# Kernel tuning notes

Hardware: AMD Instinct MI355X
Metric: run time of the kernel (lower is better)

The kernel has to match this reference:

```python
import jax, jax.numpy as jnp
import numpy as np

B, N, F, T, O, K = 4, 4000, 16, 16, 16, 3
LN_EPS = 1e-5


def setup_inputs() -> dict:
    key = jax.random.key(0)
    k = jax.random.split(key, 18)
    rn = lambda i, sh, sc=1.0: jax.random.normal(k[i], sh, dtype=jnp.float32) * np.float32(sc)
    ru = lambda i, sh: jax.random.uniform(k[i], sh, dtype=jnp.float32)
    return {
        "x": rn(0, (B, N, F, T)),
        # scale the random Laplacian so the Chebyshev recurrence stays numerically sane
        "laplacian": rn(1, (N, N), 1.0 / np.sqrt(N)),
        "W1": ru(2, (T,)),
        "W2": rn(3, (F, T)),
        "W3": ru(4, (F,)),
        "bs": ru(5, (1, N, N)),
        "Vs": ru(6, (N, N)),
        "U1": ru(7, (N,)),
        "U2": rn(8, (F, N)),
        "U3": ru(9, (F,)),
        "be": ru(10, (1, T, T)),
        "Ve": ru(11, (T, T)),
        "cheb_w": rn(12, (K, F, O), 1.0 / np.sqrt(F)),
        "time_w": rn(13, (O, F, T), 1.0 / np.sqrt(F * T)),
        "time_b": rn(14, (O,)),
        "ln_g": jnp.ones((N, O), dtype=jnp.float32),
        "ln_b": jnp.zeros((N, O), dtype=jnp.float32),
    }


def reference(x, laplacian, W1, W2, W3, bs, Vs, U1, U2, U3, be, Ve,
              cheb_w, time_w, time_b, ln_g, ln_b):
    # ---- temporal attention: E (B,T,T) ----
    # lhs[b,t] = sum_{n,f} x[b,n,f,t] * U1[n]
    t_lhs = jnp.einsum('bnft,n->bt', x, U1)
    # rhs[b,t] = sum_{n,f,g} x[b,n,f,t] * U2[g,n] * U3[g]
    t_rhs = jnp.einsum('bnft,gn,g->bt', x, U2, U3)
    t_prod = t_lhs[:, :, None] * t_rhs[:, None, :]          # (B,T,T) outer product
    E = jnp.einsum('ts,bsr->btr', Ve, jax.nn.sigmoid(t_prod + be))
    E = jax.nn.softmax(E, axis=-1)

    # apply temporal attention along the time axis: (B,N,F,T)
    x_TAt = jnp.einsum('bts,bnfs->bnft', E, x)

    # ---- spatial attention: S (B,N,N) ----
    s_lhs = jnp.einsum('bnft,t->bnf', x, W1)                 # (B,N,F)
    # faithful to the source ops (valid since F == T here)
    s_rhs = jnp.einsum('bnkt,gk,t->bng', x, W2, W3)          # (B,N,F)
    s_prod = jnp.einsum('bnf,bmf->bnm', s_lhs, s_rhs)        # (B,N,N)
    S = jnp.einsum('nm,bmk->bnk', Vs, jax.nn.sigmoid(s_prod + bs))
    S = jax.nn.softmax(S, axis=-1)

    # spatially attended features for all timesteps at once
    x_SAtt = jnp.einsum('bnm,bmft->bnft', S, x_TAt)          # (B,N,F,T)

    # ---- Chebyshev graph conv over every timestep ----
    Tx0 = x_SAtt
    out = jnp.einsum('bnft,fo->bnot', Tx0, cheb_w[0])
    Tx1 = jnp.einsum('nm,bmft->bnft', laplacian, Tx0)
    out = out + jnp.einsum('bnft,fo->bnot', Tx1, cheb_w[1])
    for kk in range(2, K):
        Tx2 = 2.0 * jnp.einsum('nm,bmft->bnft', laplacian, Tx1) - Tx0
        out = out + jnp.einsum('bnft,fo->bnot', Tx2, cheb_w[kk])
        Tx0, Tx1 = Tx1, Tx2
    spatial_gcn_avg = out.mean(axis=-1)                      # (B,N,O)

    # ---- time conv: Conv2d(in,out,kernel=(1,T)) == full contraction over (F,T) ----
    time_out = jnp.einsum('bnct,oct->bno', x, time_w) + time_b

    # ---- residual (in_channels == out_channels branch) ----
    residual = x[:, :, :, -1]                                # (B,N,O)

    y = spatial_gcn_avg + time_out + residual
    # LayerNorm over the last two dims [N, O]
    mean = y.mean(axis=(1, 2), keepdims=True)
    var = jnp.var(y, axis=(1, 2), keepdims=True)
    y = (y - mean) / jnp.sqrt(var + LN_EPS) * ln_g + ln_b
    return jax.nn.relu(y)
```

## Files before the change

### kernel.cpp

```cpp
#include <hip/hip_runtime.h>
#include <math.h>

#define Bc 4
#define Nn 4000
#define KS 4096
#define NP (16000000 + 4096)

typedef _Float16 half8 __attribute__((ext_vector_type(8)));
typedef float f32x4 __attribute__((ext_vector_type(4)));
typedef unsigned short u16x4 __attribute__((ext_vector_type(4)));

static __device__ __forceinline__ unsigned short f2h(float f) {
  _Float16 h = (_Float16)f;
  unsigned short u;
  __builtin_memcpy(&u, &h, 2);
  return u;
}
static __device__ __forceinline__ float h2f(unsigned short u) {
  _Float16 h;
  __builtin_memcpy(&h, &u, 2);
  return (float)h;
}
static __device__ __forceinline__ void gld16(const void* g, void* l) {
  __builtin_amdgcn_global_load_lds(
      (const __attribute__((address_space(1))) unsigned int*)g,
      (__attribute__((address_space(3))) unsigned int*)l, 16, 0, 0);
}

__global__ __launch_bounds__(256) void k1_trhs(
    const float* __restrict__ x, const float* __restrict__ U1,
    const float* __restrict__ U2, const float* __restrict__ U3,
    float* __restrict__ tl, float* __restrict__ tr) {
  int b = blockIdx.y;
  int tid = threadIdx.x;
  int q = tid & 3;
  int n = blockIdx.x * 64 + (tid >> 2);
  float xs[16];
#pragma unroll
  for (int t = 0; t < 16; ++t) xs[t] = 0.f;
  float c1 = 0.f, c2 = 0.f;
  if (n < Nn) {
    const float* xr = x + ((size_t)b * Nn + n) * 256 + q * 64;
#pragma unroll
    for (int f = 0; f < 4; ++f) {
#pragma unroll
      for (int qq = 0; qq < 4; ++qq) {
        float4 v = *(const float4*)(xr + f * 16 + qq * 4);
        xs[qq * 4 + 0] += v.x; xs[qq * 4 + 1] += v.y;
        xs[qq * 4 + 2] += v.z; xs[qq * 4 + 3] += v.w;
      }
    }
    c1 = U1[n];
#pragma unroll
    for (int g = 0; g < 4; ++g) {
      int gg = q * 4 + g;
      c2 += U2[(size_t)gg * Nn + n] * U3[gg];
    }
  }
#pragma unroll
  for (int m = 1; m < 4; m <<= 1) {
    c2 += __shfl_xor(c2, m, 64);
#pragma unroll
    for (int t = 0; t < 16; ++t) xs[t] += __shfl_xor(xs[t], m, 64);
  }
  float v1[4], v2[4];
#pragma unroll
  for (int i = 0; i < 4; ++i) {
    int t = q * 4 + i;
    v1[i] = c1 * xs[t];
    v2[i] = c2 * xs[t];
  }
#pragma unroll
  for (int off = 4; off < 64; off <<= 1) {
#pragma unroll
    for (int i = 0; i < 4; ++i) {
      v1[i] += __shfl_down(v1[i], off, 64);
      v2[i] += __shfl_down(v2[i], off, 64);
    }
  }
  int lane = tid & 63;
  if (lane < 4) {
#pragma unroll
    for (int i = 0; i < 4; ++i) {
      atomicAdd(&tl[b * 16 + lane * 4 + i], v1[i]);
      atomicAdd(&tr[b * 16 + lane * 4 + i], v2[i]);
    }
  }
}

__global__ __launch_bounds__(256) void k2_eattn(
    const float* __restrict__ tl, const float* __restrict__ tr,
    const float* __restrict__ be, const float* __restrict__ Ve,
    float* __restrict__ ecol) {
  int b = blockIdx.x;
  int tid = threadIdx.x;
  __shared__ float sig[256];
  __shared__ float Em[256];
  int s = tid >> 4, r = tid & 15;
  float z = tl[b * 16 + s] * tr[b * 16 + r] + be[s * 16 + r];
  sig[s * 16 + r] = 1.0f / (1.0f + __expf(-z));
  __syncthreads();
  float e = 0.f;
#pragma unroll
  for (int ss = 0; ss < 16; ++ss) e += Ve[s * 16 + ss] * sig[ss * 16 + r];
  Em[s * 16 + r] = e;
  __syncthreads();
  if (tid < 16) {
    float m = -1e30f;
#pragma unroll
    for (int rr = 0; rr < 16; ++rr) m = fmaxf(m, Em[tid * 16 + rr]);
    float ssum = 0.f;
    float ex[16];
#pragma unroll
    for (int rr = 0; rr < 16; ++rr) { ex[rr] = __expf(Em[tid * 16 + rr] - m); ssum += ex[rr]; }
    float inv = 1.0f / ssum;
#pragma unroll
    for (int rr = 0; rr < 16; ++rr) Em[tid * 16 + rr] = ex[rr] * inv;
  }
  __syncthreads();
  if (tid < 16) {
    float c = 0.f;
#pragma unroll
    for (int tt = 0; tt < 16; ++tt) c += Em[tt * 16 + tid];
    ecol[b * 16 + tid] = c;
  }
}

__global__ __launch_bounds__(256) void k3_pern(
    const float* __restrict__ x, const float* __restrict__ ecol,
    const float* __restrict__ W1, const float* __restrict__ W2,
    const float* __restrict__ W3, const float* __restrict__ time_w,
    const float* __restrict__ time_b,
    float* __restrict__ xts, float* __restrict__ slhs,
    float* __restrict__ srhs, float* __restrict__ base) {
  __shared__ float tws[4096];
  __shared__ float W1s[16], W3s[16], Ecs[16], tbs[16], W2s[256];
  int tid = threadIdx.x;
  int b = blockIdx.y;
  for (int i = tid; i < 4096; i += 256) tws[i] = time_w[i];
  W2s[tid] = W2[tid & 255];
  if (tid < 16) {
    W1s[tid] = W1[tid]; W3s[tid] = W3[tid];
    Ecs[tid] = ecol[b * 16 + tid]; tbs[tid] = time_b[tid];
  }
  __syncthreads();
  int n = blockIdx.x * 256 + tid;
  if (n >= Nn) return;
  const float* xr = x + ((size_t)b * Nn + n) * 256;
  float xtsv[16], slv[16], xw3[16], to[16], resid[16];
#pragma unroll
  for (int i = 0; i < 16; ++i) { xtsv[i] = 0; slv[i] = 0; xw3[i] = 0; to[i] = 0; }
  for (int f = 0; f < 16; ++f) {
    float xf[16];
#pragma unroll
    for (int q = 0; q < 4; ++q) {
      float4 v = *(const float4*)(xr + f * 16 + q * 4);
      xf[q * 4 + 0] = v.x; xf[q * 4 + 1] = v.y; xf[q * 4 + 2] = v.z; xf[q * 4 + 3] = v.w;
    }
    float a = 0, c = 0, d = 0;
#pragma unroll
    for (int t2 = 0; t2 < 16; ++t2) {
      a += Ecs[t2] * xf[t2];
      c += W1s[t2] * xf[t2];
      d += W3s[t2] * xf[t2];
    }
    xtsv[f] = a; slv[f] = c; xw3[f] = d; resid[f] = xf[15];
#pragma unroll
    for (int o = 0; o < 16; ++o) {
      float acc = 0;
#pragma unroll
      for (int t2 = 0; t2 < 16; ++t2) acc += tws[o * 256 + f * 16 + t2] * xf[t2];
      to[o] += acc;
    }
  }
  size_t o16 = ((size_t)b * Nn + n) * 16;
#pragma unroll
  for (int g = 0; g < 16; ++g) {
    float acc = 0;
#pragma unroll
    for (int k2 = 0; k2 < 16; ++k2) acc += W2s[g * 16 + k2] * xw3[k2];
    srhs[o16 + g] = acc;
  }
#pragma unroll
  for (int i = 0; i < 16; ++i) {
    xts[o16 + i] = xtsv[i];
    slhs[o16 + i] = slv[i];
    base[o16 + i] = to[i] + tbs[i] + resid[i];
  }
}

__global__ __launch_bounds__(256) void fconv(
    const float* __restrict__ src, unsigned short* __restrict__ dst) {
  size_t i = ((size_t)blockIdx.x * 256 + threadIdx.x) * 4;
  float4 v = *(const float4*)(src + i);
  u16x4 h;
  h.x = f2h(v.x); h.y = f2h(v.y); h.z = f2h(v.z); h.w = f2h(v.w);
  *(u16x4*)(dst + i) = h;
}

__global__ __launch_bounds__(256) void vconv2(
    const float* __restrict__ Vs, unsigned short* __restrict__ Vh) {
  int row = blockIdx.y;
  int col = blockIdx.x * 1024 + threadIdx.x * 4;
  u16x4 h;
  if (row < Nn && col < Nn) {
    float4 v = *(const float4*)(Vs + (size_t)row * Nn + col);
    h.x = f2h(v.x); h.y = f2h(v.y); h.z = f2h(v.z); h.w = f2h(v.w);
  } else {
    h.x = 0; h.y = 0; h.z = 0; h.w = 0;
  }
  *(u16x4*)(Vh + (size_t)row * KS + col) = h;
}

__global__ __launch_bounds__(256) void tsconv(
    const float* __restrict__ ts, unsigned short* __restrict__ tsT) {
  int n = blockIdx.x * 256 + threadIdx.x;
  int col = blockIdx.y;
  if (n >= Nn) return;
  int b = col >> 4, f = col & 15;
  tsT[(size_t)col * Nn + n] = f2h(ts[((size_t)b * Nn + n) * 16 + f]);
}

__global__ __launch_bounds__(256) void gemm1_P(
    const float* __restrict__ slhs, const float* __restrict__ srhs,
    const unsigned short* __restrict__ bsH, unsigned short* __restrict__ PhT, int b) {
  __shared__ float Ms[64][17];
  __shared__ float Cs[64][17];
  __shared__ float Pt[64][65];
  int tid = threadIdx.x;
  int m0 = blockIdx.y * 64, k0 = blockIdx.x * 64;
  int lr = tid >> 2, lq = (tid & 3) << 2;
  {
    int gm = m0 + lr; if (gm > Nn - 1) gm = Nn - 1;
    float4 v = *(const float4*)(slhs + ((size_t)b * Nn + gm) * 16 + lq);
    Ms[lr][lq + 0] = v.x; Ms[lr][lq + 1] = v.y; Ms[lr][lq + 2] = v.z; Ms[lr][lq + 3] = v.w;
    int gk = k0 + lr; if (gk > Nn - 1) gk = Nn - 1;
    float4 w = *(const float4*)(srhs + ((size_t)b * Nn + gk) * 16 + lq);
    Cs[lr][lq + 0] = w.x; Cs[lr][lq + 1] = w.y; Cs[lr][lq + 2] = w.z; Cs[lr][lq + 3] = w.w;
  }
  __syncthreads();
  int tx = tid & 15, ty = tid >> 4;
  float acc[4][4] = {};
#pragma unroll
  for (int f = 0; f < 16; ++f) {
    float a4[4], b4[4];
#pragma unroll
    for (int i = 0; i < 4; ++i) a4[i] = Ms[ty * 4 + i][f];
#pragma unroll
    for (int j = 0; j < 4; ++j) b4[j] = Cs[tx * 4 + j][f];
#pragma unroll
    for (int i = 0; i < 4; ++i)
#pragma unroll
      for (int j = 0; j < 4; ++j) acc[i][j] += a4[i] * b4[j];
  }
#pragma unroll
  for (int i = 0; i < 4; ++i) {
    int m = m0 + ty * 4 + i;
    int k = k0 + tx * 4;
    float bv[4] = {0.f, 0.f, 0.f, 0.f};
    if (m < Nn) {
      if (k + 3 < Nn) {
        u16x4 t4 = *(const u16x4*)(bsH + (size_t)m * Nn + k);
        bv[0] = h2f(t4.x); bv[1] = h2f(t4.y); bv[2] = h2f(t4.z); bv[3] = h2f(t4.w);
      } else {
        for (int j = 0; j < 4; ++j)
          if (k + j < Nn) bv[j] = h2f(bsH[(size_t)m * Nn + k + j]);
      }
    }
#pragma unroll
    for (int j = 0; j < 4; ++j) {
      float z = acc[i][j] + bv[j];
      Pt[ty * 4 + i][tx * 4 + j] = 1.f / (1.f + __expf(-z));
    }
  }
  __syncthreads();
#pragma unroll
  for (int i = 0; i < 4; ++i) {
    int kl = ty * 4 + i;
    int ml = tx * 4;
    int gm = m0 + ml;
    u16x4 h;
    h.x = f2h(Pt[ml + 0][kl]);
    h.y = f2h(Pt[ml + 1][kl]);
    h.z = f2h(Pt[ml + 2][kl]);
    h.w = f2h(Pt[ml + 3][kl]);
    size_t off = (size_t)(k0 + kl) * KS + gm;
    if (gm + 3 < Nn) {
      *(u16x4*)(PhT + off) = h;
    } else {
      unsigned short hv[4] = {h.x, h.y, h.z, h.w};
      for (int q = 0; q < 4; ++q)
        if (gm + q < Nn) PhT[off + q] = hv[q];
    }
  }
}

__global__ __launch_bounds__(512, 2) void gemm2_mfma(
    const unsigned short* __restrict__ Vh, const unsigned short* __restrict__ PhT,
    float* __restrict__ SP, unsigned int* __restrict__ rmaxu) {
  __shared__ unsigned short Ah[2][2][8192];
  __shared__ unsigned short Bh[2][2][8192];
  int t = threadIdx.x;
  int bid = blockIdx.x;
  int wg = (bid & 7) * 32 + (bid >> 3);
  int row0 = (wg >> 4) * 256, col0 = (wg & 15) * 256;

  int sr = t >> 2, sg = t & 3;
  int ssw = sg ^ ((t >> 3) & 3);
  size_t a0 = (size_t)(row0 + sr) * KS + ssw * 8;
  size_t a1 = (size_t)(row0 + 128 + sr) * KS + ssw * 8;
  size_t b0 = (size_t)(col0 + sr) * KS + ssw * 8;
  size_t b1 = (size_t)(col0 + 128 + sr) * KS + ssw * 8;
  int ld0 = t * 8, ld1 = 4096 + t * 8;

  int lane = t & 63, wid = t >> 6;
  int wm = (wid >> 2) * 128, wn = (wid & 3) * 64;
  int ml = lane & 15, qd = lane >> 4;
  int gr = qd ^ ((ml >> 1) & 3);
  int aro[8], bro[4];
#pragma unroll
  for (int i = 0; i < 8; ++i) aro[i] = (wm + ml + i * 16) * 32 + gr * 8;
#pragma unroll
  for (int j = 0; j < 4; ++j) bro[j] = (wn + ml + j * 16) * 32 + gr * 8;

  f32x4 acc[8][4] = {};

#define STG(P, X, bf, kh, o0, o1, kt)                          \
  do {                                                         \
    size_t c_ = (size_t)(kt) * 64 + (kh) * 32;                 \
    gld16(P + (o0) + c_, &X[bf][kh][ld0]);                     \
    gld16(P + (o1) + c_, &X[bf][kh][ld1]);                     \
  } while (0)
#define LGKM0() asm volatile("s_waitcnt lgkmcnt(0)" ::: "memory")
#define VM8()   asm volatile("s_waitcnt vmcnt(8)" ::: "memory")
#define BARR()  __builtin_amdgcn_s_barrier()

  STG(Vh, Ah, 0, 0, a0, a1, 0); STG(PhT, Bh, 0, 0, b0, b1, 0);
  STG(Vh, Ah, 0, 1, a0, a1, 0); STG(PhT, Bh, 0, 1, b0, b1, 0);
  STG(Vh, Ah, 1, 0, a0, a1, 1); STG(PhT, Bh, 1, 0, b0, b1, 1);
  STG(Vh, Ah, 1, 1, a0, a1, 1); STG(PhT, Bh, 1, 1, b0, b1, 1);
  asm volatile("s_waitcnt vmcnt(12)" ::: "memory");
  BARR();

#pragma unroll 1
  for (int G = 0; G < 64; ++G) {
    int cb = G & 1, nb = cb ^ 1;
    int tn1 = (G + 1 < 64) ? G + 1 : 63;
    int tn2 = (G + 2 < 64) ? G + 2 : 63;
    half8 av[4], bv[4];
#pragma unroll
    for (int j = 0; j < 4; ++j) bv[j] = *(const half8*)&Bh[cb][0][bro[j]];
#pragma unroll
    for (int i = 0; i < 4; ++i) av[i] = *(const half8*)&Ah[cb][0][aro[i]];
    STG(Vh, Ah, nb, 1, a0, a1, tn1);
    __builtin_amdgcn_s_setprio(1);
#pragma unroll
    for (int i = 0; i < 4; ++i)
#pragma unroll
      for (int j = 0; j < 4; ++j)
        acc[i][j] = __builtin_amdgcn_mfma_f32_16x16x32_f16(av[i], bv[j], acc[i][j], 0, 0, 0);
    __builtin_amdgcn_s_setprio(0);
    LGKM0();
    BARR();
#pragma unroll
    for (int i = 0; i < 4; ++i) av[i] = *(const half8*)&Ah[cb][0][aro[4 + i]];
    STG(PhT, Bh, nb, 1, b0, b1, tn1);
    __builtin_amdgcn_s_setprio(1);
#pragma unroll
    for (int i = 0; i < 4; ++i)
#pragma unroll
      for (int j = 0; j < 4; ++j)
        acc[4 + i][j] = __builtin_amdgcn_mfma_f32_16x16x32_f16(av[i], bv[j], acc[4 + i][j], 0, 0, 0);
    __builtin_amdgcn_s_setprio(0);
    LGKM0();
    VM8();
    BARR();
#pragma unroll
    for (int j = 0; j < 4; ++j) bv[j] = *(const half8*)&Bh[cb][1][bro[j]];
#pragma unroll
    for (int i = 0; i < 4; ++i) av[i] = *(const half8*)&Ah[cb][1][aro[i]];
    STG(Vh, Ah, cb, 0, a0, a1, tn2);
    __builtin_amdgcn_s_setprio(1);
#pragma unroll
    for (int i = 0; i < 4; ++i)
#pragma unroll
      for (int j = 0; j < 4; ++j)
        acc[i][j] = __builtin_amdgcn_mfma_f32_16x16x32_f16(av[i], bv[j], acc[i][j], 0, 0, 0);
    __builtin_amdgcn_s_setprio(0);
    LGKM0();
    BARR();
#pragma unroll
    for (int i = 0; i < 4; ++i) av[i] = *(const half8*)&Ah[cb][1][aro[4 + i]];
    STG(PhT, Bh, cb, 0, b0, b1, tn2);
    __builtin_amdgcn_s_setprio(1);
#pragma unroll
    for (int i = 0; i < 4; ++i)
#pragma unroll
      for (int j = 0; j < 4; ++j)
        acc[4 + i][j] = __builtin_amdgcn_mfma_f32_16x16x32_f16(av[i], bv[j], acc[4 + i][j], 0, 0, 0);
    __builtin_amdgcn_s_setprio(0);
    LGKM0();
    VM8();
    BARR();
  }
#undef STG
#undef LGKM0
#undef VM8
#undef BARR

#pragma unroll
  for (int i = 0; i < 8; ++i) {
#pragma unroll
    for (int r = 0; r < 4; ++r) {
      int grow = row0 + wm + i * 16 + qd * 4 + r;
      if (grow >= Nn) continue;
      float rowmax = -3.0e38f;
#pragma unroll
      for (int j = 0; j < 4; ++j) {
        int gcol = col0 + wn + j * 16 + ml;
        if (gcol < Nn) {
          float v = acc[i][j][r];
          SP[(size_t)grow * Nn + gcol] = v;
          rowmax = fmaxf(rowmax, v);
        }
      }
#pragma unroll
      for (int mk = 1; mk < 16; mk <<= 1)
        rowmax = fmaxf(rowmax, __shfl_xor(rowmax, mk, 64));
      if (ml == 0) {
        unsigned u = __float_as_uint(rowmax);
        u = (u & 0x80000000u) ? ~u : (u | 0x80000000u);
        atomicMax(rmaxu + grow, u);
      }
    }
  }
}

__global__ __launch_bounds__(256) void txsum_sp(
    const float* __restrict__ SP, const float* __restrict__ xts,
    const unsigned int* __restrict__ rmaxu, float* __restrict__ lsum,
    float* __restrict__ ts0, int b) {
  __shared__ unsigned short XT[16][824];
  int tid = threadIdx.x;
  int kbase = blockIdx.y * 800;
  for (int i4 = tid; i4 < 3200; i4 += 256) {
    int k = i4 >> 2, f4 = (i4 & 3) << 2;
    float4 v = *(const float4*)(xts + ((size_t)b * Nn + kbase + k) * 16 + f4);
    XT[f4 + 0][k] = f2h(v.x); XT[f4 + 1][k] = f2h(v.y);
    XT[f4 + 2][k] = f2h(v.z); XT[f4 + 3][k] = f2h(v.w);
  }
  __syncthreads();
  int lane = tid & 63, wid = tid >> 6;
  int ml = lane & 15, qd = lane >> 4;
  int n0 = blockIdx.x * 64 + wid * 16;
  int nr = n0 + ml;
  int nrc = nr < Nn ? nr : Nn - 1;
  unsigned u = rmaxu[nrc];
  u = (u & 0x80000000u) ? (u ^ 0x80000000u) : ~u;
  float rm = __uint_as_float(u);
  const float* spr = SP + (size_t)nrc * Nn + kbase + qd * 8;
  f32x4 acc = {0.f, 0.f, 0.f, 0.f};
  float lpart = 0.f;
#pragma unroll 1
  for (int ks = 0; ks < 25; ++ks) {
    float4 v0 = *(const float4*)(spr + ks * 32);
    float4 v1 = *(const float4*)(spr + ks * 32 + 4);
    float e0 = __expf(v0.x - rm), e1 = __expf(v0.y - rm);
    float e2 = __expf(v0.z - rm), e3 = __expf(v0.w - rm);
    float e4 = __expf(v1.x - rm), e5 = __expf(v1.y - rm);
    float e6 = __expf(v1.z - rm), e7 = __expf(v1.w - rm);
    lpart += ((e0 + e1) + (e2 + e3)) + ((e4 + e5) + (e6 + e7));
    half8 a_h, b_h;
    a_h[0] = (_Float16)e0; a_h[1] = (_Float16)e1;
    a_h[2] = (_Float16)e2; a_h[3] = (_Float16)e3;
    a_h[4] = (_Float16)e4; a_h[5] = (_Float16)e5;
    a_h[6] = (_Float16)e6; a_h[7] = (_Float16)e7;
    b_h = *(const half8*)&XT[ml][ks * 32 + qd * 8];
    acc = __builtin_amdgcn_mfma_f32_16x16x32_f16(a_h, b_h, acc, 0, 0, 0);
  }
  lpart += __shfl_xor(lpart, 16, 64);
  lpart += __shfl_xor(lpart, 32, 64);
  if (qd == 0 && nr < Nn) atomicAdd(&lsum[nr], lpart);
#pragma unroll
  for (int r = 0; r < 4; ++r) {
    int n = n0 + qd * 4 + r;
    if (n < Nn) atomicAdd(&ts0[((size_t)b * Nn + n) * 16 + ml], acc[r]);
  }
}

__global__ __launch_bounds__(256) void nrm_k(
    float* __restrict__ ts0, const float* __restrict__ lsum) {
  int tid = threadIdx.x;
  int b = blockIdx.y;
  int n = blockIdx.x * 16 + (tid >> 4);
  size_t i = ((size_t)b * Nn + n) * 16 + (tid & 15);
  ts0[i] = ts0[i] / lsum[b * Nn + n];
}

__global__ __launch_bounds__(256) void chebm(
    const unsigned short* __restrict__ lapH, const unsigned short* __restrict__ tsT,
    float* __restrict__ Cout) {
  __shared__ unsigned short Ah[64 * 32];
  __shared__ unsigned short Bh[64 * 32];
  int t = threadIdx.x;
  int row0 = blockIdx.x * 64;
  int kc0 = blockIdx.y * 25 * 32;
  int kc1 = kc0 + 25 * 32;
  int arow = row0 + (t >> 2); if (arow > Nn - 1) arow = Nn - 1;
  size_t a_base = (size_t)arow * Nn + (t & 3) * 8;
  size_t b_base = (size_t)(t >> 2) * Nn + (t & 3) * 8;

  int lane = t & 63;
  int wid = t >> 6;
  int wm = (wid >> 1) * 32, wn = (wid & 1) * 32;
  int ml = lane & 15, qd = lane >> 4;
  int aoff = (wm + ml) * 32 + qd * 8;
  int boff = (wn + ml) * 32 + qd * 8;

  f32x4 acc[2][2] = {};

  for (int k0 = kc0; k0 < kc1; k0 += 32) {
    gld16(lapH + a_base + k0, &Ah[t * 8]);
    gld16(tsT + b_base + k0, &Bh[t * 8]);
    __syncthreads();
    half8 a_h[2], b_h[2];
#pragma unroll
    for (int i = 0; i < 2; ++i) a_h[i] = *(const half8*)&Ah[aoff + i * 512];
#pragma unroll
    for (int j = 0; j < 2; ++j) b_h[j] = *(const half8*)&Bh[boff + j * 512];
#pragma unroll
    for (int i = 0; i < 2; ++i)
#pragma unroll
      for (int j = 0; j < 2; ++j)
        acc[i][j] = __builtin_amdgcn_mfma_f32_16x16x32_f16(a_h[i], b_h[j], acc[i][j], 0, 0, 0);
    __syncthreads();
  }
#pragma unroll
  for (int i = 0; i < 2; ++i)
#pragma unroll
    for (int j = 0; j < 2; ++j) {
      int gcol = wn + j * 16 + ml;
      int b = gcol >> 4, f = gcol & 15;
#pragma unroll
      for (int r = 0; r < 4; ++r) {
        int grow = row0 + wm + i * 16 + qd * 4 + r;
        if (grow < Nn) {
          size_t idx = ((size_t)b * Nn + grow) * 16 + f;
          atomicAdd(&Cout[idx], acc[i][j][r]);
        }
      }
    }
}

__global__ __launch_bounds__(256) void ky_k(
    const float* __restrict__ ts0, const float* __restrict__ ts1,
    const float* __restrict__ ts2, const float* __restrict__ cw,
    const float* __restrict__ base, float* __restrict__ ybuf,
    float* __restrict__ lnacc) {
  __shared__ float T0[256], T1[256], T2[256], CW[768];
  __shared__ float rs[256], rq[256];
  int tid = threadIdx.x;
  int b = blockIdx.y;
  size_t base_i = ((size_t)b * Nn + blockIdx.x * 16) * 16;
  T0[tid] = ts0[base_i + tid];
  T1[tid] = ts1[base_i + tid];
  T2[tid] = ts2[base_i + tid];
  for (int i = tid; i < 768; i += 256) CW[i] = cw[i];
  __syncthreads();
  int r = tid >> 4, o = tid & 15;
  float acc = 0.f;
#pragma unroll
  for (int f2 = 0; f2 < 16; ++f2) {
    float c2 = CW[512 + f2 * 16 + o];
    acc += T0[r * 16 + f2] * (CW[f2 * 16 + o] - c2);
    acc += T1[r * 16 + f2] * CW[256 + f2 * 16 + o];
    acc += (2.0f * T2[r * 16 + f2]) * c2;
  }
  float y = acc * 0.0625f + base[base_i + tid];
  ybuf[base_i + tid] = y;
  rs[tid] = y; rq[tid] = y * y;
  __syncthreads();
  for (int s2 = 128; s2 > 0; s2 >>= 1) {
    if (tid < s2) { rs[tid] += rs[tid + s2]; rq[tid] += rq[tid + s2]; }
    __syncthreads();
  }
  if (tid == 0) {
    atomicAdd(&lnacc[b * 2 + 0], rs[0]);
    atomicAdd(&lnacc[b * 2 + 1], rq[0]);
  }
}

__global__ __launch_bounds__(256) void kln_k(
    const float* __restrict__ ybuf, const float* __restrict__ lnacc,
    const float* __restrict__ lg, const float* __restrict__ lb,
    float* __restrict__ outp) {
  int tid = threadIdx.x;
  int b = blockIdx.y;
  size_t i = ((size_t)b * Nn + blockIdx.x * 16) * 16 + tid;
  size_t nz = (size_t)blockIdx.x * 256 + tid;
  const float inv = 1.0f / 64000.0f;
  float s = lnacc[b * 2 + 0], q = lnacc[b * 2 + 1];
  float mean = s * inv;
  float var = q * inv - mean * mean;
  float rstd = rsqrtf(var + 1e-5f);
  float v = (ybuf[i] - mean) * rstd * lg[nz] + lb[nz];
  outp[i] = fmaxf(v, 0.f);
}

extern "C" void kernel_launch(void* const* d_in, const int* in_sizes, int n_in,
                              void* d_out, int out_size, void* d_ws, size_t ws_size,
                              hipStream_t stream) {
  const float* x   = (const float*)d_in[0];
  const float* lap = (const float*)d_in[1];
  const float* W1  = (const float*)d_in[2];
  const float* W2  = (const float*)d_in[3];
  const float* W3  = (const float*)d_in[4];
  const float* bs  = (const float*)d_in[5];
  const float* Vs  = (const float*)d_in[6];
  const float* U1  = (const float*)d_in[7];
  const float* U2  = (const float*)d_in[8];
  const float* U3  = (const float*)d_in[9];
  const float* be  = (const float*)d_in[10];
  const float* Ve  = (const float*)d_in[11];
  const float* cw  = (const float*)d_in[12];
  const float* tw  = (const float*)d_in[13];
  const float* tb  = (const float*)d_in[14];
  const float* lg  = (const float*)d_in[15];
  const float* lb  = (const float*)d_in[16];
  float* ws = (float*)d_ws;
  float* SP = ws;
  unsigned short* Vh   = (unsigned short*)(ws + (size_t)NP);
  unsigned short* PhT  = Vh + (size_t)KS * KS;
  unsigned short* lapH = PhT + (size_t)KS * KS;
  unsigned short* bsH  = lapH + (size_t)Nn * Nn;
  unsigned short* tsT  = bsH + (size_t)Nn * Nn;
  float* xts  = (float*)(tsT + 64 * Nn + 64);
  float* slhs = xts + 256000;
  float* srhs = slhs + 256000;
  float* base = srhs + 256000;
  float* ts0  = base + 256000;
  float* ts1  = ts0 + 256000;
  float* ts2  = ts1 + 256000;
  float* ybuf = ts2 + 256000;
  float* tl   = ybuf + 256000;
  float* tr   = tl + 64;
  float* ecol = tr + 64;
  unsigned int* rmaxu = (unsigned int*)(ecol + 64);
  float* lsum = (float*)(rmaxu + Bc * Nn);
  float* lnacc = lsum + Bc * Nn;

  hipMemsetAsync(tl, 0, 128 * sizeof(float), stream);
  hipMemsetAsync(lnacc, 0, 8 * sizeof(float), stream);
  hipMemsetAsync(ts0, 0, 256000 * sizeof(float), stream);
  hipMemsetAsync(ts1, 0, 256000 * sizeof(float), stream);
  hipMemsetAsync(ts2, 0, 256000 * sizeof(float), stream);
  hipMemsetAsync(rmaxu, 0, Bc * Nn * sizeof(unsigned int), stream);
  hipMemsetAsync(lsum, 0, Bc * Nn * sizeof(float), stream);

  k1_trhs<<<dim3(63, 4), 256, 0, stream>>>(x, U1, U2, U3, tl, tr);
  k2_eattn<<<dim3(4), 256, 0, stream>>>(tl, tr, be, Ve, ecol);
  k3_pern<<<dim3(16, 4), 256, 0, stream>>>(x, ecol, W1, W2, W3, tw, tb,
                                           xts, slhs, srhs, base);
  vconv2<<<dim3(4, 4096), 256, 0, stream>>>(Vs, Vh);
  fconv<<<dim3(15625), 256, 0, stream>>>(lap, lapH);
  fconv<<<dim3(15625), 256, 0, stream>>>(bs, bsH);
  for (int b = 0; b < 4; ++b) {
    gemm1_P<<<dim3(63, 63), 256, 0, stream>>>(slhs, srhs, bsH, PhT, b);
    gemm2_mfma<<<dim3(256), 512, 0, stream>>>(Vh, PhT, SP, rmaxu + b * Nn);
    txsum_sp<<<dim3(63, 5), 256, 0, stream>>>(SP, xts, rmaxu + b * Nn,
                                              lsum + b * Nn, ts0, b);
  }
  nrm_k<<<dim3(250, 4), 256, 0, stream>>>(ts0, lsum);
  tsconv<<<dim3(16, 64), 256, 0, stream>>>(ts0, tsT);
  chebm<<<dim3(63, 5), 256, 0, stream>>>(lapH, tsT, ts1);
  tsconv<<<dim3(16, 64), 256, 0, stream>>>(ts1, tsT);
  chebm<<<dim3(63, 5), 256, 0, stream>>>(lapH, tsT, ts2);
  ky_k<<<dim3(250, 4), 256, 0, stream>>>(ts0, ts1, ts2, cw, base, ybuf, lnacc);
  kln_k<<<dim3(250, 4), 256, 0, stream>>>(ybuf, lnacc, lg, lb, (float*)d_out);
}
```

Measured before the change: 1.102 ms.

## Split per-node work across lanes, fuse conversions, double-buffer chebm loads

After: 1.074 ms. -2.5%, faster.

```diff
diff --git a/kernel.cpp b/kernel.cpp
--- a/kernel.cpp
+++ b/kernel.cpp
@@ -133,29 +133,36 @@
     const float* __restrict__ time_b,
     float* __restrict__ xts, float* __restrict__ slhs,
     float* __restrict__ srhs, float* __restrict__ base) {
-  __shared__ float tws[4096];
+  __shared__ float tws[16 * 272];
   __shared__ float W1s[16], W3s[16], Ecs[16], tbs[16], W2s[256];
   int tid = threadIdx.x;
   int b = blockIdx.y;
-  for (int i = tid; i < 4096; i += 256) tws[i] = time_w[i];
+  for (int i = tid; i < 4096; i += 256) {
+    int o = i >> 8, rem = i & 255, f = rem >> 4, t2 = rem & 15;
+    tws[o * 272 + f * 17 + t2] = time_w[i];
+  }
   W2s[tid] = W2[tid & 255];
   if (tid < 16) {
     W1s[tid] = W1[tid]; W3s[tid] = W3[tid];
     Ecs[tid] = ecol[b * 16 + tid]; tbs[tid] = time_b[tid];
   }
   __syncthreads();
-  int n = blockIdx.x * 256 + tid;
+  int q = tid & 3;
+  int n = blockIdx.x * 64 + (tid >> 2);
   if (n >= Nn) return;
-  const float* xr = x + ((size_t)b * Nn + n) * 256;
-  float xtsv[16], slv[16], xw3[16], to[16], resid[16];
-#pragma unroll
-  for (int i = 0; i < 16; ++i) { xtsv[i] = 0; slv[i] = 0; xw3[i] = 0; to[i] = 0; }
-  for (int f = 0; f < 16; ++f) {
+  const float* xr = x + ((size_t)b * Nn + n) * 256 + q * 64;
+  float xtsv[4], slv[4], xw3[4], resid[4], to[16];
+#pragma unroll
+  for (int o = 0; o < 16; ++o) to[o] = 0.f;
+#pragma unroll
+  for (int fl = 0; fl < 4; ++fl) {
+    int f = q * 4 + fl;
     float xf[16];
 #pragma unroll
-    for (int q = 0; q < 4; ++q) {
-      float4 v = *(const float4*)(xr + f * 16 + q * 4);
-      xf[q * 4 + 0] = v.x; xf[q * 4 + 1] = v.y; xf[q * 4 + 2] = v.z; xf[q * 4 + 3] = v.w;
+    for (int qq = 0; qq < 4; ++qq) {
+      float4 v = *(const float4*)(xr + fl * 16 + qq * 4);
+      xf[qq * 4 + 0] = v.x; xf[qq * 4 + 1] = v.y;
+      xf[qq * 4 + 2] = v.z; xf[qq * 4 + 3] = v.w;
     }
     float a = 0, c = 0, d = 0;
 #pragma unroll
@@ -164,34 +171,48 @@
       c += W1s[t2] * xf[t2];
       d += W3s[t2] * xf[t2];
     }
-    xtsv[f] = a; slv[f] = c; xw3[f] = d; resid[f] = xf[15];
+    xtsv[fl] = a; slv[fl] = c; xw3[fl] = d; resid[fl] = xf[15];
 #pragma unroll
     for (int o = 0; o < 16; ++o) {
       float acc = 0;
 #pragma unroll
-      for (int t2 = 0; t2 < 16; ++t2) acc += tws[o * 256 + f * 16 + t2] * xf[t2];
+      for (int t2 = 0; t2 < 16; ++t2) acc += tws[o * 272 + f * 17 + t2] * xf[t2];
       to[o] += acc;
     }
   }
-  size_t o16 = ((size_t)b * Nn + n) * 16;
+#pragma unroll
+  for (int m = 1; m < 4; m <<= 1)
+#pragma unroll
+    for (int o = 0; o < 16; ++o) to[o] += __shfl_xor(to[o], m, 64);
+  float sg[16];
 #pragma unroll
   for (int g = 0; g < 16; ++g) {
     float acc = 0;
 #pragma unroll
-    for (int k2 = 0; k2 < 16; ++k2) acc += W2s[g * 16 + k2] * xw3[k2];
-    srhs[o16 + g] = acc;
-  }
-#pragma unroll
-  for (int i = 0; i < 16; ++i) {
-    xts[o16 + i] = xtsv[i];
-    slhs[o16 + i] = slv[i];
-    base[o16 + i] = to[i] + tbs[i] + resid[i];
-  }
-}
-
-__global__ __launch_bounds__(256) void fconv(
-    const float* __restrict__ src, unsigned short* __restrict__ dst) {
+    for (int k2l = 0; k2l < 4; ++k2l) acc += W2s[g * 16 + q * 4 + k2l] * xw3[k2l];
+    sg[g] = acc;
+  }
+#pragma unroll
+  for (int m = 1; m < 4; m <<= 1)
+#pragma unroll
+    for (int g = 0; g < 16; ++g) sg[g] += __shfl_xor(sg[g], m, 64);
+  size_t o16 = ((size_t)b * Nn + n) * 16;
+#pragma unroll
+  for (int i = 0; i < 4; ++i) {
+    int idx = q * 4 + i;
+    xts[o16 + idx] = xtsv[i];
+    slhs[o16 + idx] = slv[i];
+    srhs[o16 + idx] = sg[idx];
+    base[o16 + idx] = to[idx] + tbs[idx] + resid[i];
+  }
+}
+
+__global__ __launch_bounds__(256) void fconv2(
+    const float* __restrict__ s0, const float* __restrict__ s1,
+    unsigned short* __restrict__ d0, unsigned short* __restrict__ d1) {
   size_t i = ((size_t)blockIdx.x * 256 + threadIdx.x) * 4;
+  const float* src = blockIdx.y ? s1 : s0;
+  unsigned short* dst = blockIdx.y ? d1 : d0;
   float4 v = *(const float4*)(src + i);
   u16x4 h;
   h.x = f2h(v.x); h.y = f2h(v.y); h.z = f2h(v.z); h.w = f2h(v.w);
@@ -210,6 +231,19 @@
     h.x = 0; h.y = 0; h.z = 0; h.w = 0;
   }
   *(u16x4*)(Vh + (size_t)row * KS + col) = h;
+}
+
+__global__ __launch_bounds__(256) void tsconv_n(
+    float* __restrict__ ts, const float* __restrict__ lsum,
+    unsigned short* __restrict__ tsT) {
+  int n = blockIdx.x * 256 + threadIdx.x;
+  int col = blockIdx.y;
+  if (n >= Nn) return;
+  int b = col >> 4, f = col & 15;
+  size_t i = ((size_t)b * Nn + n) * 16 + f;
+  float v = ts[i] / lsum[(size_t)b * Nn + n];
+  ts[i] = v;
+  tsT[(size_t)col * Nn + n] = f2h(v);
 }
 
 __global__ __launch_bounds__(256) void tsconv(
@@ -488,20 +522,11 @@
   }
 }
 
-__global__ __launch_bounds__(256) void nrm_k(
-    float* __restrict__ ts0, const float* __restrict__ lsum) {
-  int tid = threadIdx.x;
-  int b = blockIdx.y;
-  int n = blockIdx.x * 16 + (tid >> 4);
-  size_t i = ((size_t)b * Nn + n) * 16 + (tid & 15);
-  ts0[i] = ts0[i] / lsum[b * Nn + n];
-}
-
 __global__ __launch_bounds__(256) void chebm(
     const unsigned short* __restrict__ lapH, const unsigned short* __restrict__ tsT,
     float* __restrict__ Cout) {
-  __shared__ unsigned short Ah[64 * 32];
-  __shared__ unsigned short Bh[64 * 32];
+  __shared__ unsigned short Ah[2][2048];
+  __shared__ unsigned short Bh[2][2048];
   int t = threadIdx.x;
   int row0 = blockIdx.x * 64;
   int kc0 = blockIdx.y * 25 * 32;
@@ -519,21 +544,29 @@
 
   f32x4 acc[2][2] = {};
 
+  gld16(lapH + a_base + kc0, &Ah[0][t * 8]);
+  gld16(tsT + b_base + kc0, &Bh[0][t * 8]);
+  int cur = 0;
+#pragma unroll 1
   for (int k0 = kc0; k0 < kc1; k0 += 32) {
-    gld16(lapH + a_base + k0, &Ah[t * 8]);
-    gld16(tsT + b_base + k0, &Bh[t * 8]);
-    __syncthreads();
+    int nxt = cur ^ 1;
+    gld16(lapH + a_base + k0 + 32, &Ah[nxt][t * 8]);
+    gld16(tsT + b_base + k0 + 32, &Bh[nxt][t * 8]);
+    asm volatile("s_waitcnt vmcnt(2)" ::: "memory");
+    __builtin_amdgcn_s_barrier();
     half8 a_h[2], b_h[2];
 #pragma unroll
-    for (int i = 0; i < 2; ++i) a_h[i] = *(const half8*)&Ah[aoff + i * 512];
-#pragma unroll
-    for (int j = 0; j < 2; ++j) b_h[j] = *(const half8*)&Bh[boff + j * 512];
+    for (int i = 0; i < 2; ++i) a_h[i] = *(const half8*)&Ah[cur][aoff + i * 512];
+#pragma unroll
+    for (int j = 0; j < 2; ++j) b_h[j] = *(const half8*)&Bh[cur][boff + j * 512];
 #pragma unroll
     for (int i = 0; i < 2; ++i)
 #pragma unroll
       for (int j = 0; j < 2; ++j)
         acc[i][j] = __builtin_amdgcn_mfma_f32_16x16x32_f16(a_h[i], b_h[j], acc[i][j], 0, 0, 0);
-    __syncthreads();
+    asm volatile("s_waitcnt lgkmcnt(0)" ::: "memory");
+    __builtin_amdgcn_s_barrier();
+    cur = nxt;
   }
 #pragma unroll
   for (int i = 0; i < 2; ++i)
@@ -659,19 +692,17 @@
 
   k1_trhs<<<dim3(63, 4), 256, 0, stream>>>(x, U1, U2, U3, tl, tr);
   k2_eattn<<<dim3(4), 256, 0, stream>>>(tl, tr, be, Ve, ecol);
-  k3_pern<<<dim3(16, 4), 256, 0, stream>>>(x, ecol, W1, W2, W3, tw, tb,
+  k3_pern<<<dim3(63, 4), 256, 0, stream>>>(x, ecol, W1, W2, W3, tw, tb,
                                            xts, slhs, srhs, base);
   vconv2<<<dim3(4, 4096), 256, 0, stream>>>(Vs, Vh);
-  fconv<<<dim3(15625), 256, 0, stream>>>(lap, lapH);
-  fconv<<<dim3(15625), 256, 0, stream>>>(bs, bsH);
+  fconv2<<<dim3(15625, 2), 256, 0, stream>>>(lap, bs, lapH, bsH);
   for (int b = 0; b < 4; ++b) {
     gemm1_P<<<dim3(63, 63), 256, 0, stream>>>(slhs, srhs, bsH, PhT, b);
     gemm2_mfma<<<dim3(256), 512, 0, stream>>>(Vh, PhT, SP, rmaxu + b * Nn);
     txsum_sp<<<dim3(63, 5), 256, 0, stream>>>(SP, xts, rmaxu + b * Nn,
                                               lsum + b * Nn, ts0, b);
   }
-  nrm_k<<<dim3(250, 4), 256, 0, stream>>>(ts0, lsum);
-  tsconv<<<dim3(16, 64), 256, 0, stream>>>(ts0, tsT);
+  tsconv_n<<<dim3(16, 64), 256, 0, stream>>>(ts0, lsum, tsT);
   chebm<<<dim3(63, 5), 256, 0, stream>>>(lapH, tsT, ts1);
   tsconv<<<dim3(16, 64), 256, 0, stream>>>(ts1, tsT);
   chebm<<<dim3(63, 5), 256, 0, stream>>>(lapH, tsT, ts2);
```
